# Performance work log

Measured on AMD Instinct MI355X. Metric: run time of the kernel, lower is better.

## Reference

```python
import jax, jax.numpy as jnp
import numpy as np

NEG_SLOPE = 0.2

def _gat_conv(x, src, dst, W, a_src, a_dst, b, heads, out_ch, concat):
    N = x.shape[0]
    h = (x @ W).reshape(N, heads, out_ch)                      # [N,H,C]
    al_s = jnp.einsum('nhc,hc->nh', h, a_src)                  # [N,H]
    al_d = jnp.einsum('nhc,hc->nh', h, a_dst)
    e = jax.nn.leaky_relu(al_s[src] + al_d[dst], NEG_SLOPE)    # [E,H]
    emax = jax.ops.segment_max(e, dst, num_segments=N)         # [N,H]
    ex = jnp.exp(e - emax[dst])
    denom = jax.ops.segment_sum(ex, dst, num_segments=N)
    alpha = ex / denom[dst]                                    # [E,H]
    msg = h[src] * alpha[:, :, None]                           # [E,H,C]
    out = jax.ops.segment_sum(msg, dst, num_segments=N)        # [N,H,C]
    if concat:
        out = out.reshape(N, heads * out_ch)
    else:
        out = out.mean(axis=1)
    return out + b

def _add_self_loops(edge_index, N):
    loops = jnp.arange(N, dtype=edge_index.dtype)
    src = jnp.concatenate([edge_index[0], loops])
    dst = jnp.concatenate([edge_index[1], loops])
    return src, dst

def setup_inputs() -> dict:
    key = jax.random.key(0)
    ks = jax.random.split(key, 16)
    N, E, Fin, C, H, G, OUT = 50000, 1600000, 128, 32, 8, 256, 64
    s = 0.05
    inp = {
        'x': jax.random.normal(ks[0], (N, Fin), jnp.float32),
        'edge_index': jax.random.randint(ks[1], (2, E), 0, N, jnp.int64),
        'batch': jnp.sort(jax.random.randint(ks[2], (N,), 0, G, jnp.int64)),
        'W0': jax.random.normal(ks[3], (Fin, H * C), jnp.float32) * s,
        'a_src0': jax.random.normal(ks[4], (H, C), jnp.float32) * s,
        'a_dst0': jax.random.normal(ks[5], (H, C), jnp.float32) * s,
        'b0': jnp.zeros((H * C,), jnp.float32),
        'W1': jax.random.normal(ks[6], (H * C, H * C), jnp.float32) * s,
        'a_src1': jax.random.normal(ks[7], (H, C), jnp.float32) * s,
        'a_dst1': jax.random.normal(ks[8], (H, C), jnp.float32) * s,
        'b1': jnp.zeros((H * C,), jnp.float32),
        'W2': jax.random.normal(ks[9], (H * C, C), jnp.float32) * s,
        'a_src2': jax.random.normal(ks[10], (1, C), jnp.float32) * s,
        'a_dst2': jax.random.normal(ks[11], (1, C), jnp.float32) * s,
        'b2': jnp.zeros((C,), jnp.float32),
        'lin_w': jax.random.normal(ks[12], (C, OUT), jnp.float32) * s,
        'lin_b': jnp.zeros((OUT,), jnp.float32),
    }
    return inp

def reference(x, edge_index, batch, W0, a_src0, a_dst0, b0, W1, a_src1, a_dst1, b1,
              W2, a_src2, a_dst2, b2, lin_w, lin_b):
    N = x.shape[0]
    G = 256
    src, dst = _add_self_loops(edge_index, N)
    h = jax.nn.relu(_gat_conv(x, src, dst, W0, a_src0, a_dst0, b0, 8, 32, True))
    h = jax.nn.relu(_gat_conv(h, src, dst, W1, a_src1, a_dst1, b1, 8, 32, True))
    h = _gat_conv(h, src, dst, W2, a_src2, a_dst2, b2, 1, 32, True)  # heads=1 concat -> [N,32]
    # global mean pool over graphs
    sums = jax.ops.segment_sum(h, batch, num_segments=G)
    cnts = jax.ops.segment_sum(jnp.ones((N,), h.dtype), batch, num_segments=G)
    pooled = sums / jnp.maximum(cnts, 1.0)[:, None]
    return pooled @ lin_w + lin_b
```

## Files before the change

### kernel.cpp

```cpp
#include <hip/hip_runtime.h>
#include <hip/hip_bf16.h>


#define LRELU(x) ((x) >= 0.f ? (x) : 0.2f * (x))

typedef unsigned short ushort8 __attribute__((ext_vector_type(8)));
typedef unsigned short ushort4v __attribute__((ext_vector_type(4)));
typedef __attribute__((ext_vector_type(8))) short bf16x8;
typedef __attribute__((ext_vector_type(4))) float f32x4;

__device__ __forceinline__ float bf2f(unsigned short u) {
    return __uint_as_float(((unsigned)u) << 16);
}
__device__ __forceinline__ unsigned short f2bf(float f) {
    __hip_bfloat16 b = __float2bfloat16(f);
    return *reinterpret_cast<unsigned short*>(&b);
}
__device__ __forceinline__ void gl_lds16(const unsigned short* g, unsigned short* l) {
    __builtin_amdgcn_global_load_lds((const __attribute__((address_space(1))) void*)g,
                                     (__attribute__((address_space(3))) void*)l, 16, 0, 0);
}


__global__ void deg_kernel(const int* __restrict__ dst, int* __restrict__ deg,
                           int E, int N) {
    int i = blockIdx.x * blockDim.x + threadIdx.x;
    if (i < E) atomicAdd(&deg[dst[i]], 1);
    else if (i < E + N) atomicAdd(&deg[i - E], 1);
}

__global__ void scan_kernel(const int* __restrict__ deg, int* __restrict__ rowptr,
                            int n) {
    __shared__ int partial[1024];
    const int tid = threadIdx.x;
    const int chunk = (n + 1023) / 1024;
    const int start = min(tid * chunk, n);
    const int end = min(start + chunk, n);
    int s = 0;
    for (int i = start; i < end; i++) s += deg[i];
    partial[tid] = s;
    __syncthreads();
    for (int o = 1; o < 1024; o <<= 1) {
        int v = (tid >= o) ? partial[tid - o] : 0;
        __syncthreads();
        partial[tid] += v;
        __syncthreads();
    }
    int run = (tid == 0) ? 0 : partial[tid - 1];
    for (int i = start; i < end; i++) { rowptr[i] = run; run += deg[i]; }
    if (tid == 0) rowptr[n] = partial[1023];
}

__global__ void scatter_col_binned(const int* __restrict__ src, const int* __restrict__ dst,
                                   int* __restrict__ rowptr, int* __restrict__ col,
                                   int E, int N, int lo, int hi) {
    int i = blockIdx.x * blockDim.x + threadIdx.x;
    if (i < E) {
        int d = dst[i];
        if (d < lo || d >= hi) return;
        int pos = atomicAdd(&rowptr[d], 1);
        col[pos] = src[i];
    } else if (i < E + N) {
        int d = i - E;
        if (d < lo || d >= hi) return;
        int pos = atomicAdd(&rowptr[d], 1);
        col[pos] = d;
    }
}

__global__ void expand_dst_kernel(const int* __restrict__ rowptr, int* __restrict__ dstA,
                                  int N) {
    int n = blockIdx.x * blockDim.x + threadIdx.x;
    if (n >= N) return;
    int r0 = (n == 0) ? 0 : rowptr[n - 1];
    int r1 = rowptr[n];
    for (int p = r0; p < r1; p++) dstA[p] = n;
}

__global__ void gstart_kernel(const int* __restrict__ batch, int* __restrict__ gstart,
                              int N, int G) {
    int g = blockIdx.x * blockDim.x + threadIdx.x;
    if (g > G) return;
    int lo = 0, hi = N;
    while (lo < hi) { int mid = (lo + hi) >> 1; if (batch[mid] < g) lo = mid + 1; else hi = mid; }
    gstart[g] = lo;
}


__global__ void split_plain_kernel(const float* __restrict__ X, unsigned short* __restrict__ h,
                                   unsigned short* __restrict__ l, int n) {
    int i = blockIdx.x * blockDim.x + threadIdx.x;
    if (i >= n) return;
    float v = X[i];
    unsigned short hb = f2bf(v);
    h[i] = hb;
    l[i] = f2bf(v - bf2f(hb));
}

__global__ void splitT_kernel(const float* __restrict__ W, unsigned short* __restrict__ th,
                              unsigned short* __restrict__ tl, int K, int N) {
    int i = blockIdx.x * blockDim.x + threadIdx.x;
    if (i >= N * K) return;
    int n = i / K, k = i - n * K;
    float v = W[(size_t)k * N + n];
    unsigned short hb = f2bf(v);
    th[i] = hb;
    tl[i] = f2bf(v - bf2f(hb));
}


template <int BM, int BN, int WM, int WN>
__global__ __launch_bounds__(256)
void gemm_mfma_v2(const unsigned short* __restrict__ Ah, const unsigned short* __restrict__ Al,
                  const unsigned short* __restrict__ Bth, const unsigned short* __restrict__ Btl,
                  unsigned short* __restrict__ Cc, int M, int N, int K) {
    constexpr int BK = 32;
    constexpr int MT = WM / 16, NT = WN / 16;
    constexpr int NWX = BN / WN;
    __shared__ __attribute__((aligned(16))) unsigned short Ha[BM][BK];
    __shared__ __attribute__((aligned(16))) unsigned short La[BM][BK];
    __shared__ __attribute__((aligned(16))) unsigned short Hb[BN][BK];
    __shared__ __attribute__((aligned(16))) unsigned short Lb[BN][BK];
    const int tid = threadIdx.x;
    const int lane = tid & 63;
    const int wave = tid >> 6;
    const int wx = wave % NWX, wy = wave / NWX;
    const int by = blockIdx.y * BM;
    const int bx = blockIdx.x * BN;
    const int r16 = lane & 15, kg = lane >> 4;
    const int srow = lane >> 2, sslot = lane & 3;

    f32x4 acc[MT][NT];
#pragma unroll
    for (int i = 0; i < MT; i++)
#pragma unroll
        for (int j = 0; j < NT; j++) acc[i][j] = (f32x4){0.f, 0.f, 0.f, 0.f};

    for (int k0 = 0; k0 < K; k0 += BK) {
        for (int t = wave; t < BM / 16; t += 4) {
            int gm = by + t * 16 + srow;
            if (gm >= M) gm = M - 1;
            const size_t goff = (size_t)gm * K + k0 + sslot * 8;
            gl_lds16(Ah + goff, &Ha[t * 16][0]);
            gl_lds16(Al + goff, &La[t * 16][0]);
        }
        for (int t = wave; t < BN / 16; t += 4) {
            int gn = bx + t * 16 + srow;
            const size_t goff = (size_t)gn * K + k0 + sslot * 8;
            gl_lds16(Bth + goff, &Hb[t * 16][0]);
            gl_lds16(Btl + goff, &Lb[t * 16][0]);
        }
        __syncthreads();
        bf16x8 bh[NT], bl[NT];
#pragma unroll
        for (int j = 0; j < NT; j++) {
            bh[j] = *(const bf16x8*)&Hb[wx * WN + j * 16 + r16][kg * 8];
            bl[j] = *(const bf16x8*)&Lb[wx * WN + j * 16 + r16][kg * 8];
        }
#pragma unroll
        for (int i = 0; i < MT; i++) {
            bf16x8 ah = *(const bf16x8*)&Ha[wy * WM + i * 16 + r16][kg * 8];
            bf16x8 al2 = *(const bf16x8*)&La[wy * WM + i * 16 + r16][kg * 8];
#pragma unroll
            for (int j = 0; j < NT; j++) {
                acc[i][j] = __builtin_amdgcn_mfma_f32_16x16x32_bf16(ah, bh[j], acc[i][j], 0, 0, 0);
                acc[i][j] = __builtin_amdgcn_mfma_f32_16x16x32_bf16(ah, bl[j], acc[i][j], 0, 0, 0);
                acc[i][j] = __builtin_amdgcn_mfma_f32_16x16x32_bf16(al2, bh[j], acc[i][j], 0, 0, 0);
            }
        }
        __syncthreads();
    }
#pragma unroll
    for (int i = 0; i < MT; i++) {
#pragma unroll
        for (int r = 0; r < 4; r++) {
            int gm = by + wy * WM + i * 16 + kg * 4 + r;
            if (gm >= M) continue;
#pragma unroll
            for (int j = 0; j < NT; j++) {
                int gn = bx + wx * WN + j * 16 + r16;
                Cc[(size_t)gm * N + gn] = f2bf(acc[i][j][r]);
            }
        }
    }
}


template <int H, int C>
__global__ void al_bf16(const unsigned short* __restrict__ hfeat, const float* __restrict__ a_src,
                        const float* __restrict__ a_dst, float* __restrict__ als,
                        float* __restrict__ ald, int N) {
    int i = blockIdx.x * blockDim.x + threadIdx.x;
    if (i >= N * H) return;
    int n = i / H, h = i % H;
    const unsigned short* hp = hfeat + (size_t)n * H * C + h * C;
    float s1 = 0.f, s2 = 0.f;
    for (int c0 = 0; c0 < C; c0 += 8) {
        ushort8 v = *(const ushort8*)(hp + c0);
#pragma unroll
        for (int k = 0; k < 8; k++) {
            float f = bf2f(v[k]);
            s1 += f * a_src[h * C + c0 + k];
            s2 += f * a_dst[h * C + c0 + k];
        }
    }
    als[i] = s1;
    ald[i] = s2;
}


__global__ void edge_w_pair(const float* __restrict__ als, const float* __restrict__ ald,
                            const int* __restrict__ col, const int* __restrict__ dstA,
                            unsigned int* __restrict__ wts2, int Etot) {
    int i = blockIdx.x * blockDim.x + threadIdx.x;
    if (i >= Etot * 4) return;
    int pos = i >> 2, hp = i & 3;
    int s = col[pos], d = dstA[pos];
    float2 a = *(const float2*)&als[(size_t)s * 8 + hp * 2];
    float2 b = *(const float2*)&ald[(size_t)d * 8 + hp * 2];
    float e0 = a.x + b.x; e0 = LRELU(e0);
    float e1 = a.y + b.y; e1 = LRELU(e1);
    unsigned lo = f2bf(__expf(e0));
    unsigned hi = f2bf(__expf(e1));
    wts2[i] = lo | (hi << 16);
}

__global__ void edge_w_h1(const float* __restrict__ als, const float* __restrict__ ald,
                          const int* __restrict__ col, const int* __restrict__ dstA,
                          unsigned short* __restrict__ wts, int Etot) {
    int i = blockIdx.x * blockDim.x + threadIdx.x;
    if (i >= Etot) return;
    int s = col[i], d = dstA[i];
    float e = als[s] + ald[d];
    e = LRELU(e);
    wts[i] = f2bf(__expf(e));
}


__global__ __launch_bounds__(256)
void gat_agg_w8(const unsigned short* __restrict__ hfeat,
                const unsigned short* __restrict__ wts,
                const int* __restrict__ rowptr,
                const int* __restrict__ col,
                const float* __restrict__ bias,
                unsigned short* __restrict__ outH, unsigned short* __restrict__ outL,
                int N) {
    constexpr int CAP = 128;
    const int wid = threadIdx.x >> 6;
    const int lane = threadIdx.x & 63;
    const int n = blockIdx.x * 4 + wid;
    __shared__ float se_all[4][CAP * 8];
    __shared__ int scol_all[4][CAP];
    if (n >= N) return;
    float* se = se_all[wid];
    int* scol = scol_all[wid];

    const int r0 = (n == 0) ? 0 : rowptr[n - 1];
    const int deg = rowptr[n] - r0;
    const int dh8 = deg * 8;
    const size_t wbase = (size_t)r0 * 8;
    const int dcap = min(deg, CAP);

    for (int j = lane; j < dcap; j += 64) scol[j] = col[r0 + j];

    float p0 = 0.f, p1 = 0.f, p2 = 0.f, p3 = 0.f, p4 = 0.f, p5 = 0.f, p6 = 0.f, p7 = 0.f;
    for (int base = 0; base < dh8; base += 512) {
        int idx = base + lane * 8;
        if (idx < dh8) {
            ushort8 v = *(const ushort8*)&wts[wbase + idx];
            float f0 = bf2f(v[0]), f1 = bf2f(v[1]), f2 = bf2f(v[2]), f3 = bf2f(v[3]);
            float f4 = bf2f(v[4]), f5 = bf2f(v[5]), f6 = bf2f(v[6]), f7 = bf2f(v[7]);
            p0 += f0; p1 += f1; p2 += f2; p3 += f3;
            p4 += f4; p5 += f5; p6 += f6; p7 += f7;
            if (idx < CAP * 8) {
                *(float4*)&se[idx] = (float4){f0, f1, f2, f3};
                *(float4*)&se[idx + 4] = (float4){f4, f5, f6, f7};
            }
        }
    }
#pragma unroll
    for (int m = 1; m < 64; m <<= 1) {
        p0 += __shfl_xor(p0, m); p1 += __shfl_xor(p1, m);
        p2 += __shfl_xor(p2, m); p3 += __shfl_xor(p3, m);
        p4 += __shfl_xor(p4, m); p5 += __shfl_xor(p5, m);
        p6 += __shfl_xor(p6, m); p7 += __shfl_xor(p7, m);
    }
    const int q = lane >> 3;
    float S = (q == 0) ? p0 : (q == 1) ? p1 : (q == 2) ? p2 : (q == 3) ? p3
            : (q == 4) ? p4 : (q == 5) ? p5 : (q == 6) ? p6 : p7;
    const float sinv = 1.0f / S;

    const int cb = lane * 4;
    float a0 = 0.f, a1 = 0.f, a2 = 0.f, a3 = 0.f;
    int j = 0;
    for (; j + 3 < dcap; j += 4) {
        int s0 = __builtin_amdgcn_readfirstlane(scol[j]);
        int s1 = __builtin_amdgcn_readfirstlane(scol[j + 1]);
        int s2 = __builtin_amdgcn_readfirstlane(scol[j + 2]);
        int s3 = __builtin_amdgcn_readfirstlane(scol[j + 3]);
        ushort4v v0 = *(const ushort4v*)(hfeat + (size_t)s0 * 256 + cb);
        ushort4v v1 = *(const ushort4v*)(hfeat + (size_t)s1 * 256 + cb);
        ushort4v v2 = *(const ushort4v*)(hfeat + (size_t)s2 * 256 + cb);
        ushort4v v3 = *(const ushort4v*)(hfeat + (size_t)s3 * 256 + cb);
        float w0 = se[j * 8 + q];
        float w1 = se[j * 8 + 8 + q];
        float w2 = se[j * 8 + 16 + q];
        float w3 = se[j * 8 + 24 + q];
        a0 += bf2f(v0[0]) * w0; a1 += bf2f(v0[1]) * w0; a2 += bf2f(v0[2]) * w0; a3 += bf2f(v0[3]) * w0;
        a0 += bf2f(v1[0]) * w1; a1 += bf2f(v1[1]) * w1; a2 += bf2f(v1[2]) * w1; a3 += bf2f(v1[3]) * w1;
        a0 += bf2f(v2[0]) * w2; a1 += bf2f(v2[1]) * w2; a2 += bf2f(v2[2]) * w2; a3 += bf2f(v2[3]) * w2;
        a0 += bf2f(v3[0]) * w3; a1 += bf2f(v3[1]) * w3; a2 += bf2f(v3[2]) * w3; a3 += bf2f(v3[3]) * w3;
    }
    for (; j < dcap; j++) {
        int s0 = __builtin_amdgcn_readfirstlane(scol[j]);
        ushort4v v0 = *(const ushort4v*)(hfeat + (size_t)s0 * 256 + cb);
        float w0 = se[j * 8 + q];
        a0 += bf2f(v0[0]) * w0; a1 += bf2f(v0[1]) * w0; a2 += bf2f(v0[2]) * w0; a3 += bf2f(v0[3]) * w0;
    }
    for (; j < deg; j++) {
        int s0 = col[r0 + j];
        float w0 = bf2f(wts[wbase + (size_t)j * 8 + q]);
        ushort4v v0 = *(const ushort4v*)(hfeat + (size_t)s0 * 256 + cb);
        a0 += bf2f(v0[0]) * w0; a1 += bf2f(v0[1]) * w0; a2 += bf2f(v0[2]) * w0; a3 += bf2f(v0[3]) * w0;
    }

    float4 b4 = *(const float4*)&bias[cb];
    float o0 = fmaxf(a0 * sinv + b4.x, 0.f);
    float o1 = fmaxf(a1 * sinv + b4.y, 0.f);
    float o2 = fmaxf(a2 * sinv + b4.z, 0.f);
    float o3 = fmaxf(a3 * sinv + b4.w, 0.f);
    unsigned short h0 = f2bf(o0), h1 = f2bf(o1), h2 = f2bf(o2), h3 = f2bf(o3);
    const size_t ob = (size_t)n * 256 + cb;
    *(ushort4v*)&outH[ob] = (ushort4v){h0, h1, h2, h3};
    *(ushort4v*)&outL[ob] = (ushort4v){f2bf(o0 - bf2f(h0)), f2bf(o1 - bf2f(h1)),
                                       f2bf(o2 - bf2f(h2)), f2bf(o3 - bf2f(h3))};
}


__global__ __launch_bounds__(64)
void gat_agg_h1(const unsigned short* __restrict__ hfeat,
                const unsigned short* __restrict__ wts,
                const int* __restrict__ rowptr, const int* __restrict__ col,
                const float* __restrict__ bias, float* __restrict__ out, int N) {
    constexpr int HC = 32, VEC = 8, TPE = 4, NG = 16, CAP = 128;
    const int n = blockIdx.x;
    const int tid = threadIdx.x;
    const int r0 = (n == 0) ? 0 : rowptr[n - 1];
    const int deg = rowptr[n] - r0;

    __shared__ float se[CAP];
    __shared__ float sacc[NG][HC + 4];
    __shared__ float ssum_s;

    const size_t wbase = (size_t)r0;
    float lsum = 0.f;
    for (int idx = tid; idx < deg; idx += 64) {
        float v = bf2f(wts[wbase + idx]);
        if (idx < CAP) se[idx] = v;
        lsum += v;
    }
#pragma unroll
    for (int off = 1; off < 64; off <<= 1) lsum += __shfl_xor(lsum, off);
    if (tid == 0) ssum_s = lsum;

    const int g = tid / TPE;
    const int c = tid % TPE;
    float acc[VEC] = {};
    int j = g;
    for (; j + NG < deg && j + NG <= CAP; j += 2 * NG) {
        int s0 = col[r0 + j];
        int s1 = col[r0 + j + NG];
        float w0 = se[j];
        float w1 = se[j + NG];
        ushort8 v0 = *(const ushort8*)(hfeat + (size_t)s0 * HC + c * VEC);
        ushort8 v1 = *(const ushort8*)(hfeat + (size_t)s1 * HC + c * VEC);
#pragma unroll
        for (int k = 0; k < VEC; k++) acc[k] += bf2f(v0[k]) * w0;
#pragma unroll
        for (int k = 0; k < VEC; k++) acc[k] += bf2f(v1[k]) * w1;
    }
    for (; j < deg; j += NG) {
        int s0 = col[r0 + j];
        float w0 = (j < CAP) ? se[j] : bf2f(wts[wbase + j]);
        ushort8 v0 = *(const ushort8*)(hfeat + (size_t)s0 * HC + c * VEC);
#pragma unroll
        for (int k = 0; k < VEC; k++) acc[k] += bf2f(v0[k]) * w0;
    }
    *(float4*)&sacc[g][c * VEC] = (float4){acc[0], acc[1], acc[2], acc[3]};
    *(float4*)&sacc[g][c * VEC + 4] = (float4){acc[4], acc[5], acc[6], acc[7]};
    __syncthreads();

    if (tid < HC) {
        float v = 0.f;
#pragma unroll
        for (int gg = 0; gg < NG; gg++) v += sacc[gg][tid];
        v = v / ssum_s + bias[tid];
        out[(size_t)n * HC + tid] = v;
    }
}


__global__ __launch_bounds__(256)
void pool_final_kernel(const float* __restrict__ h, const int* __restrict__ gstart,
                       const float* __restrict__ lin_w, const float* __restrict__ lin_b,
                       float* __restrict__ out) {
    const int g = blockIdx.x;
    const int tid = threadIdx.x;
    const int n0 = gstart[g], n1 = gstart[g + 1];
    const int r = tid >> 5, c = tid & 31;
    __shared__ float pp[4][32];
    __shared__ float pm[32];
    float acc = 0.f;
    for (int n = n0 + r; n < n1; n += 8) acc += h[(size_t)n * 32 + c];
    acc += __shfl_xor(acc, 32);
    if ((tid & 63) < 32) pp[tid >> 6][c] = acc;
    __syncthreads();
    if (tid < 32) {
        float s = pp[0][tid] + pp[1][tid] + pp[2][tid] + pp[3][tid];
        pm[tid] = s / fmaxf((float)(n1 - n0), 1.f);
    }
    __syncthreads();
    if (tid < 64) {
        float a = lin_b[tid];
#pragma unroll 8
        for (int cc = 0; cc < 32; cc++) a += pm[cc] * lin_w[cc * 64 + tid];
        out[(size_t)g * 64 + tid] = a;
    }
}


extern "C" void kernel_launch(void* const* d_in, const int* in_sizes, int n_in,
                              void* d_out, int out_size, void* d_ws, size_t ws_size,
                              hipStream_t stream) {
    const float* x     = (const float*)d_in[0];
    const int*   ei    = (const int*)d_in[1];
    const int*   batch = (const int*)d_in[2];
    const float* W0    = (const float*)d_in[3];
    const float* a_s0  = (const float*)d_in[4];
    const float* a_d0  = (const float*)d_in[5];
    const float* b0    = (const float*)d_in[6];
    const float* W1    = (const float*)d_in[7];
    const float* a_s1  = (const float*)d_in[8];
    const float* a_d1  = (const float*)d_in[9];
    const float* b1    = (const float*)d_in[10];
    const float* W2    = (const float*)d_in[11];
    const float* a_s2  = (const float*)d_in[12];
    const float* a_d2  = (const float*)d_in[13];
    const float* b2    = (const float*)d_in[14];
    const float* lin_w = (const float*)d_in[15];
    const float* lin_b = (const float*)d_in[16];

    const int N = in_sizes[0] / 128;
    const int E = in_sizes[1] / 2;
    const int G = 256;
    const int Etot = E + N;
    const int* src = ei;
    const int* dst = ei + E;

    char* w = (char*)d_ws;
    size_t off = 0;
    auto alloc = [&](size_t bytes) -> void* {
        void* p = (void*)(w + off);
        off += (bytes + 255) & ~(size_t)255;
        return p;
    };
    int* deg    = (int*)alloc((size_t)N * 4);
    int* rowptr = (int*)alloc((size_t)(N + 1) * 4);
    int* colA   = (int*)alloc((size_t)Etot * 4);
    int* dstA   = (int*)alloc((size_t)Etot * 4);
    int* gstart = (int*)alloc((size_t)(G + 1) * 4);
    float* als  = (float*)alloc((size_t)N * 8 * 4);
    float* ald  = (float*)alloc((size_t)N * 8 * 4);
    unsigned short* hb  = (unsigned short*)alloc((size_t)N * 256 * 2);
    unsigned short* wts = (unsigned short*)alloc((size_t)Etot * 8 * 2);
    unsigned short* g0h = (unsigned short*)alloc((size_t)N * 256 * 2);
    unsigned short* g0l = (unsigned short*)alloc((size_t)N * 256 * 2);
    float* out2 = (float*)alloc((size_t)N * 32 * 4);
    unsigned short* w0h = (unsigned short*)alloc((size_t)128 * 256 * 2);
    unsigned short* w0l = (unsigned short*)alloc((size_t)128 * 256 * 2);
    unsigned short* w1h = (unsigned short*)alloc((size_t)256 * 256 * 2);
    unsigned short* w1l = (unsigned short*)alloc((size_t)256 * 256 * 2);
    unsigned short* w2h = (unsigned short*)alloc((size_t)256 * 32 * 2);
    unsigned short* w2l = (unsigned short*)alloc((size_t)256 * 32 * 2);
    unsigned short* xh = g0h;
    unsigned short* xl = g0h + (size_t)N * 128;

    hipMemsetAsync(deg, 0, (size_t)N * 4, stream);

    deg_kernel<<<(Etot + 255) / 256, 256, 0, stream>>>(dst, deg, E, N);
    scan_kernel<<<1, 1024, 0, stream>>>(deg, rowptr, N);
    for (int p = 0; p < 4; p++) {
        int lo = (int)((size_t)N * p / 4);
        int hi = (int)((size_t)N * (p + 1) / 4);
        scatter_col_binned<<<(Etot + 255) / 256, 256, 0, stream>>>(src, dst, rowptr, colA, E, N, lo, hi);
    }
    expand_dst_kernel<<<(N + 255) / 256, 256, 0, stream>>>(rowptr, dstA, N);
    gstart_kernel<<<2, 256, 0, stream>>>(batch, gstart, N, G);

    split_plain_kernel<<<(N * 128 + 255) / 256, 256, 0, stream>>>(x, xh, xl, N * 128);
    splitT_kernel<<<(128 * 256 + 255) / 256, 256, 0, stream>>>(W0, w0h, w0l, 128, 256);
    splitT_kernel<<<(256 * 256 + 255) / 256, 256, 0, stream>>>(W1, w1h, w1l, 256, 256);
    splitT_kernel<<<(256 * 32 + 255) / 256, 256, 0, stream>>>(W2, w2h, w2l, 256, 32);

    const int MB = (N + 127) / 128;

    gemm_mfma_v2<128, 128, 64, 64><<<dim3(2, MB), 256, 0, stream>>>(xh, xl, w0h, w0l, hb, N, 256, 128);
    al_bf16<8, 32><<<(N * 8 + 255) / 256, 256, 0, stream>>>(hb, a_s0, a_d0, als, ald, N);
    edge_w_pair<<<((size_t)Etot * 4 + 255) / 256, 256, 0, stream>>>(als, ald, colA, dstA, (unsigned int*)wts, Etot);
    gat_agg_w8<<<(N + 3) / 4, 256, 0, stream>>>(hb, wts, rowptr, colA, b0, g0h, g0l, N);

    gemm_mfma_v2<128, 128, 64, 64><<<dim3(2, MB), 256, 0, stream>>>(g0h, g0l, w1h, w1l, hb, N, 256, 256);
    al_bf16<8, 32><<<(N * 8 + 255) / 256, 256, 0, stream>>>(hb, a_s1, a_d1, als, ald, N);
    edge_w_pair<<<((size_t)Etot * 4 + 255) / 256, 256, 0, stream>>>(als, ald, colA, dstA, (unsigned int*)wts, Etot);
    gat_agg_w8<<<(N + 3) / 4, 256, 0, stream>>>(hb, wts, rowptr, colA, b1, g0h, g0l, N);

    gemm_mfma_v2<128, 32, 32, 32><<<dim3(1, MB), 256, 0, stream>>>(g0h, g0l, w2h, w2l, hb, N, 32, 256);
    al_bf16<1, 32><<<(N + 255) / 256, 256, 0, stream>>>(hb, a_s2, a_d2, als, ald, N);
    edge_w_h1<<<(Etot + 255) / 256, 256, 0, stream>>>(als, ald, colA, dstA, wts, Etot);
    gat_agg_h1<<<N, 64, 0, stream>>>(hb, wts, rowptr, colA, b2, out2, N);

    pool_final_kernel<<<G, 256, 0, stream>>>(out2, gstart, lin_w, lin_b, (float*)d_out);
}
```

Before: 678.7 us.

## Widen gather unroll, rewrite single-head aggregation as wave-per-node, halve scatter passes

The 8-head aggregation loop now unrolls eight neighbor gathers at a time and accumulates with packed two-wide float math, using bit masks instead of per-element bf16 conversion, to expose more memory parallelism. The single-head aggregation kernel is replaced by one wavefront per node, four nodes per block. It stages column indices and weights in LDS and has 8 edge slots of 8 channel lanes each, reducing with shuffles instead of an LDS reduction and barrier. The binned column scatter runs in 2 passes instead of 4, trading fewer launches and edge rereads for less locality per pass. Register pressure rises with the wider unroll.

After: 685.5 us. Within noise of the previous version (+1.0%).

```diff
diff --git a/kernel.cpp b/kernel.cpp
--- a/kernel.cpp
+++ b/kernel.cpp
@@ -8,6 +8,7 @@
 typedef unsigned short ushort4v __attribute__((ext_vector_type(4)));
 typedef __attribute__((ext_vector_type(8))) short bf16x8;
 typedef __attribute__((ext_vector_type(4))) float f32x4;
+typedef __attribute__((ext_vector_type(2))) float f32x2;
 
 __device__ __forceinline__ float bf2f(unsigned short u) {
     return __uint_as_float(((unsigned)u) << 16);
@@ -291,44 +292,47 @@
     const float sinv = 1.0f / S;
 
     const int cb = lane * 4;
-    float a0 = 0.f, a1 = 0.f, a2 = 0.f, a3 = 0.f;
+    f32x2 acc01 = {0.f, 0.f}, acc23 = {0.f, 0.f};
     int j = 0;
-    for (; j + 3 < dcap; j += 4) {
-        int s0 = __builtin_amdgcn_readfirstlane(scol[j]);
-        int s1 = __builtin_amdgcn_readfirstlane(scol[j + 1]);
-        int s2 = __builtin_amdgcn_readfirstlane(scol[j + 2]);
-        int s3 = __builtin_amdgcn_readfirstlane(scol[j + 3]);
-        ushort4v v0 = *(const ushort4v*)(hfeat + (size_t)s0 * 256 + cb);
-        ushort4v v1 = *(const ushort4v*)(hfeat + (size_t)s1 * 256 + cb);
-        ushort4v v2 = *(const ushort4v*)(hfeat + (size_t)s2 * 256 + cb);
-        ushort4v v3 = *(const ushort4v*)(hfeat + (size_t)s3 * 256 + cb);
-        float w0 = se[j * 8 + q];
-        float w1 = se[j * 8 + 8 + q];
-        float w2 = se[j * 8 + 16 + q];
-        float w3 = se[j * 8 + 24 + q];
-        a0 += bf2f(v0[0]) * w0; a1 += bf2f(v0[1]) * w0; a2 += bf2f(v0[2]) * w0; a3 += bf2f(v0[3]) * w0;
-        a0 += bf2f(v1[0]) * w1; a1 += bf2f(v1[1]) * w1; a2 += bf2f(v1[2]) * w1; a3 += bf2f(v1[3]) * w1;
-        a0 += bf2f(v2[0]) * w2; a1 += bf2f(v2[1]) * w2; a2 += bf2f(v2[2]) * w2; a3 += bf2f(v2[3]) * w2;
-        a0 += bf2f(v3[0]) * w3; a1 += bf2f(v3[1]) * w3; a2 += bf2f(v3[2]) * w3; a3 += bf2f(v3[3]) * w3;
+    for (; j + 7 < dcap; j += 8) {
+        int s[8];
+#pragma unroll
+        for (int u = 0; u < 8; u++) s[u] = __builtin_amdgcn_readfirstlane(scol[j + u]);
+        uint2 d[8];
+#pragma unroll
+        for (int u = 0; u < 8; u++) d[u] = *(const uint2*)(hfeat + (size_t)s[u] * 256 + cb);
+#pragma unroll
+        for (int u = 0; u < 8; u++) {
+            float w = se[(j + u) * 8 + q];
+            f32x2 wp = {w, w};
+            acc01 += (f32x2){__uint_as_float(d[u].x << 16),
+                             __uint_as_float(d[u].x & 0xffff0000u)} * wp;
+            acc23 += (f32x2){__uint_as_float(d[u].y << 16),
+                             __uint_as_float(d[u].y & 0xffff0000u)} * wp;
+        }
     }
     for (; j < dcap; j++) {
         int s0 = __builtin_amdgcn_readfirstlane(scol[j]);
-        ushort4v v0 = *(const ushort4v*)(hfeat + (size_t)s0 * 256 + cb);
-        float w0 = se[j * 8 + q];
-        a0 += bf2f(v0[0]) * w0; a1 += bf2f(v0[1]) * w0; a2 += bf2f(v0[2]) * w0; a3 += bf2f(v0[3]) * w0;
+        uint2 d = *(const uint2*)(hfeat + (size_t)s0 * 256 + cb);
+        float w = se[j * 8 + q];
+        f32x2 wp = {w, w};
+        acc01 += (f32x2){__uint_as_float(d.x << 16), __uint_as_float(d.x & 0xffff0000u)} * wp;
+        acc23 += (f32x2){__uint_as_float(d.y << 16), __uint_as_float(d.y & 0xffff0000u)} * wp;
     }
     for (; j < deg; j++) {
         int s0 = col[r0 + j];
-        float w0 = bf2f(wts[wbase + (size_t)j * 8 + q]);
-        ushort4v v0 = *(const ushort4v*)(hfeat + (size_t)s0 * 256 + cb);
-        a0 += bf2f(v0[0]) * w0; a1 += bf2f(v0[1]) * w0; a2 += bf2f(v0[2]) * w0; a3 += bf2f(v0[3]) * w0;
+        float w = bf2f(wts[wbase + (size_t)j * 8 + q]);
+        uint2 d = *(const uint2*)(hfeat + (size_t)s0 * 256 + cb);
+        f32x2 wp = {w, w};
+        acc01 += (f32x2){__uint_as_float(d.x << 16), __uint_as_float(d.x & 0xffff0000u)} * wp;
+        acc23 += (f32x2){__uint_as_float(d.y << 16), __uint_as_float(d.y & 0xffff0000u)} * wp;
     }
 
     float4 b4 = *(const float4*)&bias[cb];
-    float o0 = fmaxf(a0 * sinv + b4.x, 0.f);
-    float o1 = fmaxf(a1 * sinv + b4.y, 0.f);
-    float o2 = fmaxf(a2 * sinv + b4.z, 0.f);
-    float o3 = fmaxf(a3 * sinv + b4.w, 0.f);
+    float o0 = fmaxf(acc01.x * sinv + b4.x, 0.f);
+    float o1 = fmaxf(acc01.y * sinv + b4.y, 0.f);
+    float o2 = fmaxf(acc23.x * sinv + b4.z, 0.f);
+    float o3 = fmaxf(acc23.y * sinv + b4.w, 0.f);
     unsigned short h0 = f2bf(o0), h1 = f2bf(o1), h2 = f2bf(o2), h3 = f2bf(o3);
     const size_t ob = (size_t)n * 256 + cb;
     *(ushort4v*)&outH[ob] = (ushort4v){h0, h1, h2, h3};
@@ -337,65 +341,72 @@
 }
 
 
-__global__ __launch_bounds__(64)
-void gat_agg_h1(const unsigned short* __restrict__ hfeat,
-                const unsigned short* __restrict__ wts,
-                const int* __restrict__ rowptr, const int* __restrict__ col,
-                const float* __restrict__ bias, float* __restrict__ out, int N) {
-    constexpr int HC = 32, VEC = 8, TPE = 4, NG = 16, CAP = 128;
-    const int n = blockIdx.x;
-    const int tid = threadIdx.x;
+__global__ __launch_bounds__(256)
+void gat_agg_h1w(const unsigned short* __restrict__ hfeat,
+                 const unsigned short* __restrict__ wts,
+                 const int* __restrict__ rowptr, const int* __restrict__ col,
+                 const float* __restrict__ bias, float* __restrict__ out, int N) {
+    constexpr int CAP = 256;
+    const int wid = threadIdx.x >> 6;
+    const int lane = threadIdx.x & 63;
+    const int n = blockIdx.x * 4 + wid;
+    __shared__ float sw_all[4][CAP];
+    __shared__ int scol_all[4][CAP];
+    if (n >= N) return;
+    float* sw = sw_all[wid];
+    int* scol = scol_all[wid];
+
     const int r0 = (n == 0) ? 0 : rowptr[n - 1];
     const int deg = rowptr[n] - r0;
-
-    __shared__ float se[CAP];
-    __shared__ float sacc[NG][HC + 4];
-    __shared__ float ssum_s;
-
-    const size_t wbase = (size_t)r0;
+    const int dcap = min(deg, CAP);
+
     float lsum = 0.f;
-    for (int idx = tid; idx < deg; idx += 64) {
-        float v = bf2f(wts[wbase + idx]);
-        if (idx < CAP) se[idx] = v;
+    for (int idx = lane; idx < deg; idx += 64) {
+        float v = bf2f(wts[r0 + idx]);
+        if (idx < CAP) { sw[idx] = v; scol[idx] = col[r0 + idx]; }
         lsum += v;
     }
 #pragma unroll
-    for (int off = 1; off < 64; off <<= 1) lsum += __shfl_xor(lsum, off);
-    if (tid == 0) ssum_s = lsum;
-
-    const int g = tid / TPE;
-    const int c = tid % TPE;
-    float acc[VEC] = {};
-    int j = g;
-    for (; j + NG < deg && j + NG <= CAP; j += 2 * NG) {
-        int s0 = col[r0 + j];
-        int s1 = col[r0 + j + NG];
-        float w0 = se[j];
-        float w1 = se[j + NG];
-        ushort8 v0 = *(const ushort8*)(hfeat + (size_t)s0 * HC + c * VEC);
-        ushort8 v1 = *(const ushort8*)(hfeat + (size_t)s1 * HC + c * VEC);
-#pragma unroll
-        for (int k = 0; k < VEC; k++) acc[k] += bf2f(v0[k]) * w0;
-#pragma unroll
-        for (int k = 0; k < VEC; k++) acc[k] += bf2f(v1[k]) * w1;
-    }
-    for (; j < deg; j += NG) {
-        int s0 = col[r0 + j];
-        float w0 = (j < CAP) ? se[j] : bf2f(wts[wbase + j]);
-        ushort8 v0 = *(const ushort8*)(hfeat + (size_t)s0 * HC + c * VEC);
-#pragma unroll
-        for (int k = 0; k < VEC; k++) acc[k] += bf2f(v0[k]) * w0;
-    }
-    *(float4*)&sacc[g][c * VEC] = (float4){acc[0], acc[1], acc[2], acc[3]};
-    *(float4*)&sacc[g][c * VEC + 4] = (float4){acc[4], acc[5], acc[6], acc[7]};
-    __syncthreads();
-
-    if (tid < HC) {
-        float v = 0.f;
-#pragma unroll
-        for (int gg = 0; gg < NG; gg++) v += sacc[gg][tid];
-        v = v / ssum_s + bias[tid];
-        out[(size_t)n * HC + tid] = v;
+    for (int m = 1; m < 64; m <<= 1) lsum += __shfl_xor(lsum, m);
+    const float sinv = 1.0f / lsum;
+
+    const int slot = lane >> 3, ch = lane & 7;
+    f32x2 acc01 = {0.f, 0.f}, acc23 = {0.f, 0.f};
+    for (int j = 0; j < dcap; j += 8) {
+        int e = j + slot;
+        int ec = min(e, dcap - 1);
+        int s = scol[ec];
+        float w = (e < dcap) ? sw[ec] : 0.f;
+        uint2 d = *(const uint2*)(hfeat + (size_t)s * 32 + ch * 4);
+        f32x2 wp = {w, w};
+        acc01 += (f32x2){__uint_as_float(d.x << 16), __uint_as_float(d.x & 0xffff0000u)} * wp;
+        acc23 += (f32x2){__uint_as_float(d.y << 16), __uint_as_float(d.y & 0xffff0000u)} * wp;
+    }
+    for (int j = CAP; j < deg; j += 8) {
+        int e = j + slot;
+        int ec = min(e, deg - 1);
+        int s = col[r0 + ec];
+        float w = (e < deg) ? bf2f(wts[r0 + ec]) : 0.f;
+        uint2 d = *(const uint2*)(hfeat + (size_t)s * 32 + ch * 4);
+        f32x2 wp = {w, w};
+        acc01 += (f32x2){__uint_as_float(d.x << 16), __uint_as_float(d.x & 0xffff0000u)} * wp;
+        acc23 += (f32x2){__uint_as_float(d.y << 16), __uint_as_float(d.y & 0xffff0000u)} * wp;
+    }
+#pragma unroll
+    for (int m = 8; m < 64; m <<= 1) {
+        acc01.x += __shfl_xor(acc01.x, m);
+        acc01.y += __shfl_xor(acc01.y, m);
+        acc23.x += __shfl_xor(acc23.x, m);
+        acc23.y += __shfl_xor(acc23.y, m);
+    }
+    if (slot == 0) {
+        float4 b4 = *(const float4*)&bias[ch * 4];
+        float4 o;
+        o.x = acc01.x * sinv + b4.x;
+        o.y = acc01.y * sinv + b4.y;
+        o.z = acc23.x * sinv + b4.z;
+        o.w = acc23.y * sinv + b4.w;
+        *(float4*)&out[(size_t)n * 32 + ch * 4] = o;
     }
 }
 
@@ -489,9 +500,9 @@
 
     deg_kernel<<<(Etot + 255) / 256, 256, 0, stream>>>(dst, deg, E, N);
     scan_kernel<<<1, 1024, 0, stream>>>(deg, rowptr, N);
-    for (int p = 0; p < 4; p++) {
-        int lo = (int)((size_t)N * p / 4);
-        int hi = (int)((size_t)N * (p + 1) / 4);
+    for (int p = 0; p < 2; p++) {
+        int lo = (int)((size_t)N * p / 2);
+        int hi = (int)((size_t)N * (p + 1) / 2);
         scatter_col_binned<<<(Etot + 255) / 256, 256, 0, stream>>>(src, dst, rowptr, colA, E, N, lo, hi);
     }
     expand_dst_kernel<<<(N + 255) / 256, 256, 0, stream>>>(rowptr, dstA, N);
@@ -517,7 +528,7 @@
     gemm_mfma_v2<128, 32, 32, 32><<<dim3(1, MB), 256, 0, stream>>>(g0h, g0l, w2h, w2l, hb, N, 32, 256);
     al_bf16<1, 32><<<(N + 255) / 256, 256, 0, stream>>>(hb, a_s2, a_d2, als, ald, N);
     edge_w_h1<<<(Etot + 255) / 256, 256, 0, stream>>>(als, ald, colA, dstA, wts, Etot);
-    gat_agg_h1<<<N, 64, 0, stream>>>(hb, wts, rowptr, colA, b2, out2, N);
+    gat_agg_h1w<<<(N + 3) / 4, 256, 0, stream>>>(hb, wts, rowptr, colA, b2, out2, N);
 
     pool_final_kernel<<<G, 256, 0, stream>>>(out2, gstart, lin_w, lin_b, (float*)d_out);
 }
```
